# Kernel optimization log

Hardware: AMD Instinct MI355X
Metric: run time of the kernel (lower is better)

## Reference

```python
import jax, jax.numpy as jnp
import numpy as np

B, C_IN, T = 4, 256, 8192
LAYERS, STACKS = 24, 4
RES, GATE, SKIP, K = 128, 256, 128, 3
LPS = LAYERS // STACKS  # layers per stack -> dilation = 2**(i % LPS)
SQRT_HALF = 0.7071067811865476


def setup_inputs() -> dict:
    key = jax.random.key(0)
    ks = jax.random.split(key, 14)
    s = 0.08  # small init so the 24-layer stack stays well-scaled
    inp = {
        "x": jax.random.normal(ks[0], (B, C_IN, T), jnp.float32),
        "first_w": jax.random.normal(ks[1], (RES, C_IN), jnp.float32) * s,
        "first_b": jnp.zeros((RES,), jnp.float32),
        "conv_w": jax.random.normal(ks[2], (LAYERS, GATE, RES, K), jnp.float32) * s,
        "conv_b": jnp.zeros((LAYERS, GATE), jnp.float32),
        "out_w": jax.random.normal(ks[3], (LAYERS, RES, GATE // 2), jnp.float32) * s,
        "out_b": jnp.zeros((LAYERS, RES), jnp.float32),
        "skip_w": jax.random.normal(ks[4], (LAYERS, SKIP, GATE // 2), jnp.float32) * s,
        "skip_b": jnp.zeros((LAYERS, SKIP), jnp.float32),
        "last1_w": jax.random.normal(ks[5], (SKIP, SKIP), jnp.float32) * s,
        "last1_b": jnp.zeros((SKIP,), jnp.float32),
        "last2_w": jax.random.normal(ks[6], (C_IN, SKIP), jnp.float32) * s,
        "last2_b": jnp.zeros((C_IN,), jnp.float32),
    }
    return inp


def _conv1x1(w, b, h):
    # h: [B, C, T], w: [O, C]
    return jnp.einsum('oc,bct->bot', w, h) + b[None, :, None]


def _causal_dilated_conv(h, w, b, dilation):
    # left pad == torch symmetric pad (k-1)*d followed by crop to first T (causal)
    pad = (K - 1) * dilation
    hp = jnp.pad(h, ((0, 0), (0, 0), (pad, 0)))
    y = jax.lax.conv_general_dilated(
        hp, w, window_strides=(1,), padding='VALID',
        rhs_dilation=(dilation,), dimension_numbers=('NCH', 'OIH', 'NCH'))
    return y + b[None, :, None]


def reference(x, first_w, first_b, conv_w, conv_b, out_w, out_b,
              skip_w, skip_b, last1_w, last1_b, last2_w, last2_b):
    h = _conv1x1(first_w, first_b, x)  # [B, RES, T]
    skips = jnp.zeros((x.shape[0], SKIP, x.shape[-1]), h.dtype)
    for i in range(LAYERS):
        d = 2 ** (i % LPS)
        y = _causal_dilated_conv(h, conv_w[i], conv_b[i], d)  # [B, GATE, T]
        a, g = jnp.split(y, 2, axis=1)
        z = jnp.tanh(a) * jax.nn.sigmoid(g)  # gated tanh*sigmoid
        skips = skips + _conv1x1(skip_w[i], skip_b[i], z)
        h = (_conv1x1(out_w[i], out_b[i], z) + h) * SQRT_HALF  # residual
    skips = skips * (1.0 / LAYERS) ** 0.5
    out = jax.nn.relu(skips)
    out = jax.nn.relu(_conv1x1(last1_w, last1_b, out))
    out = _conv1x1(last2_w, last2_b, out)  # logits [B, 256, T]
    return out
```

## Files before the change

### kernel.cpp

```cpp
#include <hip/hip_runtime.h>

#define B 4
#define CIN 256
#define T 8192
#define NL 24
#define SH 0.70710678118654752f
#define SKIP_SCALE 0.20412414523193150f

typedef unsigned short u16;
typedef __attribute__((ext_vector_type(4))) float f32x4;
typedef __attribute__((ext_vector_type(8))) short s16x8;
typedef __attribute__((ext_vector_type(4))) short s16x4;

__device__ inline u16 f2bf(float f) {
  unsigned u = __float_as_uint(f);
  return (u16)((u + 0x7fffu + ((u >> 16) & 1u)) >> 16);
}
__device__ inline float gate_fn(float a, float g) {
  float e2 = __expf(-2.f * fabsf(a));
  float th = (1.f - e2) * __builtin_amdgcn_rcpf(1.f + e2);
  float sg = __builtin_amdgcn_rcpf(1.f + __expf(-g));
  return copysignf(th, a) * sg;
}

__global__ void cvt_all(const float* __restrict__ conv_w, const float* __restrict__ skip_w,
                        const float* __restrict__ out_w, const float* __restrict__ first_w,
                        const float* __restrict__ last1_w, const float* __restrict__ last2_w,
                        u16* __restrict__ wcv, u16* __restrict__ wso, u16* __restrict__ wf,
                        u16* __restrict__ w1, u16* __restrict__ w2) {
  int i = blockIdx.x * 256 + threadIdx.x;
  if (i < 2359296) {
    int c = i & 127, o = (i >> 7) & 255, kk = (i >> 15) % 3, l = (i >> 15) / 3;
    wcv[i] = f2bf(conv_w[(((size_t)l * 256 + o) * 128 + c) * 3 + kk]);
    return;
  }
  i -= 2359296;
  if (i < 786432) {
    int c = i & 127, r = (i >> 7) & 255, l = i >> 15;
    float v = (r < 128) ? skip_w[((size_t)l * 128 + r) * 128 + c]
                        : out_w[((size_t)l * 128 + (r - 128)) * 128 + c];
    wso[i] = f2bf(v);
    return;
  }
  i -= 786432;
  if (i < 32768) { wf[i] = f2bf(first_w[i]); return; }
  i -= 32768;
  if (i < 16384) { w1[i] = f2bf(last1_w[i]); return; }
  i -= 16384;
  if (i < 32768) { w2[i] = f2bf(last2_w[i]); return; }
}
__global__ void sumsb_kernel(const float* __restrict__ sb, float* __restrict__ dst) {
  int c = threadIdx.x;
  float s = 0.f;
  for (int l = 0; l < NL; l++) s += sb[l * 128 + c];
  dst[c] = s;
}

__global__ __launch_bounds__(256, 2)
void first_kernel(const float* __restrict__ x, const u16* __restrict__ wf,
                  const float* __restrict__ fb, float* __restrict__ hf) {
  __shared__ u16 xT[64 * 256];
  const int tid = threadIdx.x, wv = tid >> 6, lane = tid & 63, lo = lane & 15, hi = lane >> 4;
  const int t0 = blockIdx.x * 64, b = blockIdx.y;

  #pragma unroll
  for (int it = 0; it < 16; it++) {
    int idx = tid + it * 256;
    int c = idx >> 4, t4 = (idx & 15) << 2;
    f32x4 v = *(const f32x4*)(x + ((size_t)b * CIN + c) * T + t0 + t4);
    #pragma unroll
    for (int i = 0; i < 4; i++) {
      int t = t4 + i;
      *(u16*)((char*)xT + t * 512 + ((c * 2) ^ ((t & 7) << 4))) = f2bf(v[i]);
    }
  }
  __syncthreads();

  f32x4 acc[2][4];
  #pragma unroll
  for (int m = 0; m < 2; m++)
    #pragma unroll
    for (int n = 0; n < 4; n++) acc[m][n] = (f32x4){0.f, 0.f, 0.f, 0.f};
  #pragma unroll
  for (int s = 0; s < 8; s++) {
    s16x8 af[2], bf[4];
    #pragma unroll
    for (int m = 0; m < 2; m++)
      af[m] = *(const s16x8*)(wf + (size_t)(wv * 32 + m * 16 + lo) * CIN + s * 32 + hi * 8);
    #pragma unroll
    for (int n = 0; n < 4; n++) {
      int t = n * 16 + lo;
      bf[n] = *(const s16x8*)((const char*)xT + t * 512 + ((s * 64 + hi * 16) ^ ((t & 7) << 4)));
    }
    #pragma unroll
    for (int m = 0; m < 2; m++)
      #pragma unroll
      for (int n = 0; n < 4; n++)
        acc[m][n] = __builtin_amdgcn_mfma_f32_16x16x32_bf16(af[m], bf[n], acc[m][n], 0, 0, 0);
  }
  #pragma unroll
  for (int m = 0; m < 2; m++) {
    int c0 = wv * 32 + m * 16 + hi * 4;
    f32x4 bv = *(const f32x4*)(fb + c0);
    #pragma unroll
    for (int n = 0; n < 4; n++) {
      int t = n * 16 + lo;
      *(f32x4*)(hf + ((size_t)b * T + t0 + t) * 128 + c0) = acc[m][n] + bv;
    }
  }
}

__global__ __launch_bounds__(512, 4)
void pair_kernel(const float* __restrict__ hf_in, float* __restrict__ hf_out,
                 float* __restrict__ skip,
                 const u16* __restrict__ wc1, const float* __restrict__ cb1,
                 const u16* __restrict__ ws1, const float* __restrict__ ob1,
                 const u16* __restrict__ wc2, const float* __restrict__ cb2,
                 const u16* __restrict__ ws2, const float* __restrict__ ob2,
                 int d1, int d2, int first) {
  extern __shared__ u16 lds[];
  u16* h_s = lds;
  u16* zh  = lds + 160 * 128;
  const int tid = threadIdx.x, wv = tid >> 6, lane = tid & 63, lo = lane & 15, hi = lane >> 4;
  const int tj = blockIdx.x, b = blockIdx.y, t0 = tj * 64;
  const int R0 = 128 + 2 * d1;

  for (int p = tid; p < R0 * 32; p += 512) {
    int j0 = p >> 5, cq = p & 31;
    int t = t0 - 64 - 2 * d1 + j0;
    f32x4 v = (f32x4){0.f, 0.f, 0.f, 0.f};
    if (t >= 0) v = *(const f32x4*)(hf_in + ((size_t)b * T + t) * 128 + cq * 4);
    s16x4 pk;
    #pragma unroll
    for (int j = 0; j < 4; j++) pk[j] = (short)f2bf(v[j]);
    *(s16x4*)((char*)h_s + j0 * 256 + ((cq * 8) ^ (((j0 + 64 - 2 * d1) & 7) << 4))) = pk;
  }
  __syncthreads();

  f32x4 A[2][8];
  const int oa = wv * 16, og = 128 + wv * 16;

  #pragma unroll
  for (int m = 0; m < 2; m++)
    #pragma unroll
    for (int n = 0; n < 8; n++) A[m][n] = (f32x4){0.f, 0.f, 0.f, 0.f};
  #pragma unroll
  for (int k = 0; k < 3; k++) {
    const int st = ((lo + (k + 6) * d1) & 7) << 4;
    const int jb = k * d1;
    #pragma unroll
    for (int s = 0; s < 4; s++) {
      s16x8 af0 = *(const s16x8*)(wc1 + ((size_t)(k * 256 + oa + lo)) * 128 + s * 32 + hi * 8);
      s16x8 af1 = *(const s16x8*)(wc1 + ((size_t)(k * 256 + og + lo)) * 128 + s * 32 + hi * 8);
      const int cb_ = s * 64 + hi * 16;
      #pragma unroll
      for (int h2 = 0; h2 < 2; h2++) {
        s16x8 bf[4];
        #pragma unroll
        for (int nn = 0; nn < 4; nn++) {
          int j0 = (h2 * 4 + nn) * 16 + lo + jb;
          bf[nn] = *(const s16x8*)((const char*)h_s + j0 * 256 + (cb_ ^ st));
        }
        #pragma unroll
        for (int nn = 0; nn < 4; nn++) {
          A[0][h2 * 4 + nn] = __builtin_amdgcn_mfma_f32_16x16x32_bf16(af0, bf[nn], A[0][h2 * 4 + nn], 0, 0, 0);
          A[1][h2 * 4 + nn] = __builtin_amdgcn_mfma_f32_16x16x32_bf16(af1, bf[nn], A[1][h2 * 4 + nn], 0, 0, 0);
        }
      }
    }
  }
  {
    f32x4 ba = *(const f32x4*)(cb1 + oa + hi * 4);
    f32x4 bg = *(const f32x4*)(cb1 + og + hi * 4);
    #pragma unroll
    for (int n = 0; n < 8; n++) {
      int u = n * 16 + lo;
      s16x4 pk;
      #pragma unroll
      for (int j = 0; j < 4; j++)
        pk[j] = (short)f2bf(gate_fn(A[0][n][j] + ba[j], A[1][n][j] + bg[j]));
      *(s16x4*)((char*)zh + u * 256 + (((oa + hi * 4) * 2) ^ ((lo & 7) << 4))) = pk;
    }
  }
  __syncthreads();

  const int ro = wv * 32;
  if (wv < 4) {
    #pragma unroll
    for (int m = 0; m < 2; m++)
      #pragma unroll
      for (int nn = 0; nn < 4; nn++) A[m][nn + 4] = (f32x4){0.f, 0.f, 0.f, 0.f};
    #pragma unroll
    for (int s = 0; s < 4; s++) {
      s16x8 af0 = *(const s16x8*)(ws1 + (size_t)(ro + lo) * 128 + s * 32 + hi * 8);
      s16x8 af1 = *(const s16x8*)(ws1 + (size_t)(ro + 16 + lo) * 128 + s * 32 + hi * 8);
      const int cb_ = s * 64 + hi * 16;
      s16x8 bf[4];
      #pragma unroll
      for (int nn = 0; nn < 4; nn++) {
        int u = (nn + 4) * 16 + lo;
        bf[nn] = *(const s16x8*)((const char*)zh + u * 256 + (cb_ ^ ((lo & 7) << 4)));
      }
      #pragma unroll
      for (int nn = 0; nn < 4; nn++) {
        A[0][nn + 4] = __builtin_amdgcn_mfma_f32_16x16x32_bf16(af0, bf[nn], A[0][nn + 4], 0, 0, 0);
        A[1][nn + 4] = __builtin_amdgcn_mfma_f32_16x16x32_bf16(af1, bf[nn], A[1][nn + 4], 0, 0, 0);
      }
    }
  } else {
    #pragma unroll
    for (int m = 0; m < 2; m++)
      #pragma unroll
      for (int n = 0; n < 8; n++) A[m][n] = (f32x4){0.f, 0.f, 0.f, 0.f};
    #pragma unroll
    for (int s = 0; s < 4; s++) {
      s16x8 af0 = *(const s16x8*)(ws1 + (size_t)(ro + lo) * 128 + s * 32 + hi * 8);
      s16x8 af1 = *(const s16x8*)(ws1 + (size_t)(ro + 16 + lo) * 128 + s * 32 + hi * 8);
      const int cb_ = s * 64 + hi * 16;
      #pragma unroll
      for (int h2 = 0; h2 < 2; h2++) {
        s16x8 bf[4];
        #pragma unroll
        for (int nn = 0; nn < 4; nn++) {
          int u = (h2 * 4 + nn) * 16 + lo;
          bf[nn] = *(const s16x8*)((const char*)zh + u * 256 + (cb_ ^ ((lo & 7) << 4)));
        }
        #pragma unroll
        for (int nn = 0; nn < 4; nn++) {
          A[0][h2 * 4 + nn] = __builtin_amdgcn_mfma_f32_16x16x32_bf16(af0, bf[nn], A[0][h2 * 4 + nn], 0, 0, 0);
          A[1][h2 * 4 + nn] = __builtin_amdgcn_mfma_f32_16x16x32_bf16(af1, bf[nn], A[1][h2 * 4 + nn], 0, 0, 0);
        }
      }
    }
    #pragma unroll
    for (int m = 0; m < 2; m++) {
      int c0 = (wv - 4) * 32 + m * 16 + hi * 4;
      f32x4 ob4 = *(const f32x4*)(ob1 + c0);
      #pragma unroll
      for (int n = 0; n < 8; n++) {
        int u = n * 16 + lo;
        int t_out = t0 - 64 + u;
        f32x4 h0 = (f32x4){0.f, 0.f, 0.f, 0.f};
        if (t_out >= 0) h0 = *(const f32x4*)(hf_in + ((size_t)b * T + t_out) * 128 + c0);
        f32x4 h1 = (A[m][n] + ob4 + h0) * SH;
        if (t_out < 0) h1 = (f32x4){0.f, 0.f, 0.f, 0.f};
        A[m][n] = h1;
        s16x4 pk;
        #pragma unroll
        for (int j = 0; j < 4; j++) pk[j] = (short)f2bf(h1[j]);
        *(s16x4*)((char*)h_s + u * 256 + ((c0 * 2) ^ ((lo & 7) << 4))) = pk;
      }
    }
  }
  __syncthreads();

  #pragma unroll
  for (int m = 0; m < 2; m++)
    #pragma unroll
    for (int n = 0; n < 4; n++) A[m][n] = (f32x4){0.f, 0.f, 0.f, 0.f};
  #pragma unroll
  for (int k = 0; k < 3; k++) {
    const int st = ((lo + (k + 6) * d2) & 7) << 4;
    const int jb2 = 64 - 2 * d2 + k * d2;
    #pragma unroll
    for (int s = 0; s < 4; s++) {
      s16x8 af0 = *(const s16x8*)(wc2 + ((size_t)(k * 256 + oa + lo)) * 128 + s * 32 + hi * 8);
      s16x8 af1 = *(const s16x8*)(wc2 + ((size_t)(k * 256 + og + lo)) * 128 + s * 32 + hi * 8);
      const int cb_ = s * 64 + hi * 16;
      s16x8 bf[4];
      #pragma unroll
      for (int nn = 0; nn < 4; nn++) {
        int j1 = nn * 16 + lo + jb2;
        bf[nn] = *(const s16x8*)((const char*)h_s + j1 * 256 + (cb_ ^ st));
      }
      #pragma unroll
      for (int nn = 0; nn < 4; nn++) {
        A[0][nn] = __builtin_amdgcn_mfma_f32_16x16x32_bf16(af0, bf[nn], A[0][nn], 0, 0, 0);
        A[1][nn] = __builtin_amdgcn_mfma_f32_16x16x32_bf16(af1, bf[nn], A[1][nn], 0, 0, 0);
      }
    }
  }
  {
    f32x4 ba = *(const f32x4*)(cb2 + oa + hi * 4);
    f32x4 bg = *(const f32x4*)(cb2 + og + hi * 4);
    #pragma unroll
    for (int n = 0; n < 4; n++) {
      int u = n * 16 + lo;
      s16x4 pk;
      #pragma unroll
      for (int j = 0; j < 4; j++)
        pk[j] = (short)f2bf(gate_fn(A[0][n][j] + ba[j], A[1][n][j] + bg[j]));
      *(s16x4*)((char*)zh + u * 256 + (((oa + hi * 4) * 2) ^ ((lo & 7) << 4))) = pk;
    }
  }
  __syncthreads();

  if (wv < 4) {
    #pragma unroll
    for (int s = 0; s < 4; s++) {
      s16x8 af0 = *(const s16x8*)(ws2 + (size_t)(ro + lo) * 128 + s * 32 + hi * 8);
      s16x8 af1 = *(const s16x8*)(ws2 + (size_t)(ro + 16 + lo) * 128 + s * 32 + hi * 8);
      const int cb_ = s * 64 + hi * 16;
      s16x8 bf[4];
      #pragma unroll
      for (int nn = 0; nn < 4; nn++) {
        int u = nn * 16 + lo;
        bf[nn] = *(const s16x8*)((const char*)zh + u * 256 + (cb_ ^ ((lo & 7) << 4)));
      }
      #pragma unroll
      for (int nn = 0; nn < 4; nn++) {
        A[0][nn + 4] = __builtin_amdgcn_mfma_f32_16x16x32_bf16(af0, bf[nn], A[0][nn + 4], 0, 0, 0);
        A[1][nn + 4] = __builtin_amdgcn_mfma_f32_16x16x32_bf16(af1, bf[nn], A[1][nn + 4], 0, 0, 0);
      }
    }
    #pragma unroll
    for (int m = 0; m < 2; m++) {
      int c0 = ro + m * 16 + hi * 4;
      #pragma unroll
      for (int n = 0; n < 4; n++) {
        int t = t0 + n * 16 + lo;
        size_t off = ((size_t)b * T + t) * 128 + c0;
        f32x4 r = A[m][n + 4];
        if (!first) r += *(const f32x4*)(skip + off);
        *(f32x4*)(skip + off) = r;
      }
    }
  } else {
    #pragma unroll
    for (int m = 0; m < 2; m++)
      #pragma unroll
      for (int n = 0; n < 4; n++) A[m][n] = (f32x4){0.f, 0.f, 0.f, 0.f};
    #pragma unroll
    for (int s = 0; s < 4; s++) {
      s16x8 af0 = *(const s16x8*)(ws2 + (size_t)(ro + lo) * 128 + s * 32 + hi * 8);
      s16x8 af1 = *(const s16x8*)(ws2 + (size_t)(ro + 16 + lo) * 128 + s * 32 + hi * 8);
      const int cb_ = s * 64 + hi * 16;
      s16x8 bf[4];
      #pragma unroll
      for (int nn = 0; nn < 4; nn++) {
        int u = nn * 16 + lo;
        bf[nn] = *(const s16x8*)((const char*)zh + u * 256 + (cb_ ^ ((lo & 7) << 4)));
      }
      #pragma unroll
      for (int nn = 0; nn < 4; nn++) {
        A[0][nn] = __builtin_amdgcn_mfma_f32_16x16x32_bf16(af0, bf[nn], A[0][nn], 0, 0, 0);
        A[1][nn] = __builtin_amdgcn_mfma_f32_16x16x32_bf16(af1, bf[nn], A[1][nn], 0, 0, 0);
      }
    }
    #pragma unroll
    for (int m = 0; m < 2; m++) {
      int c0 = (wv - 4) * 32 + m * 16 + hi * 4;
      f32x4 ob4 = *(const f32x4*)(ob2 + c0);
      #pragma unroll
      for (int n = 0; n < 4; n++) {
        int t = t0 + n * 16 + lo;
        f32x4 h2v = (A[m][n] + ob4 + A[m][n + 4]) * SH;
        *(f32x4*)(hf_out + ((size_t)b * T + t) * 128 + c0) = h2v;
      }
    }
  }
}

__global__ __launch_bounds__(256, 2)
void head_kernel(const float* __restrict__ skip, const float* __restrict__ sumsb,
                 const u16* __restrict__ w1, const float* __restrict__ b1v,
                 const u16* __restrict__ w2, const float* __restrict__ b2v,
                 float* __restrict__ out) {
  __shared__ u16 sT[64 * 128];
  __shared__ u16 s1T[64 * 128];
  const int tid = threadIdx.x, wv = tid >> 6, lane = tid & 63, lo = lane & 15, hi = lane >> 4;
  const int t0 = blockIdx.x * 64, b = blockIdx.y;

  #pragma unroll
  for (int it = 0; it < 8; it++) {
    int p = tid + it * 256;
    int t = p >> 5, cq = p & 31;
    f32x4 v = *(const f32x4*)(skip + ((size_t)b * T + t0 + t) * 128 + cq * 4);
    f32x4 sb4 = *(const f32x4*)(sumsb + cq * 4);
    s16x4 pk;
    #pragma unroll
    for (int j = 0; j < 4; j++) pk[j] = (short)f2bf(fmaxf((v[j] + sb4[j]) * SKIP_SCALE, 0.f));
    *(s16x4*)((char*)sT + t * 256 + ((cq * 8) ^ ((t & 7) << 4))) = pk;
  }
  __syncthreads();
  {
    f32x4 acc[2][4];
    #pragma unroll
    for (int m = 0; m < 2; m++)
      #pragma unroll
      for (int n = 0; n < 4; n++) acc[m][n] = (f32x4){0.f, 0.f, 0.f, 0.f};
    #pragma unroll
    for (int s = 0; s < 4; s++) {
      s16x8 af0 = *(const s16x8*)(w1 + (size_t)(wv * 32 + lo) * 128 + s * 32 + hi * 8);
      s16x8 af1 = *(const s16x8*)(w1 + (size_t)(wv * 32 + 16 + lo) * 128 + s * 32 + hi * 8);
      #pragma unroll
      for (int n = 0; n < 4; n++) {
        int t = n * 16 + lo;
        s16x8 bf = *(const s16x8*)((const char*)sT + t * 256 + ((s * 64 + hi * 16) ^ ((t & 7) << 4)));
        acc[0][n] = __builtin_amdgcn_mfma_f32_16x16x32_bf16(af0, bf, acc[0][n], 0, 0, 0);
        acc[1][n] = __builtin_amdgcn_mfma_f32_16x16x32_bf16(af1, bf, acc[1][n], 0, 0, 0);
      }
    }
    #pragma unroll
    for (int m = 0; m < 2; m++) {
      int c0 = wv * 32 + m * 16 + hi * 4;
      f32x4 bv = *(const f32x4*)(b1v + c0);
      #pragma unroll
      for (int n = 0; n < 4; n++) {
        int t = n * 16 + lo;
        s16x4 pk;
        #pragma unroll
        for (int j = 0; j < 4; j++) pk[j] = (short)f2bf(fmaxf(acc[m][n][j] + bv[j], 0.f));
        *(s16x4*)((char*)s1T + t * 256 + ((c0 * 2) ^ ((t & 7) << 4))) = pk;
      }
    }
  }
  __syncthreads();
  {
    f32x4 acc[4][4];
    #pragma unroll
    for (int m = 0; m < 4; m++)
      #pragma unroll
      for (int n = 0; n < 4; n++) acc[m][n] = (f32x4){0.f, 0.f, 0.f, 0.f};
    #pragma unroll
    for (int s = 0; s < 4; s++) {
      s16x8 af[4];
      #pragma unroll
      for (int m = 0; m < 4; m++)
        af[m] = *(const s16x8*)(w2 + (size_t)(wv * 64 + m * 16 + lo) * 128 + s * 32 + hi * 8);
      #pragma unroll
      for (int n = 0; n < 4; n++) {
        int t = n * 16 + lo;
        s16x8 bf = *(const s16x8*)((const char*)s1T + t * 256 + ((s * 64 + hi * 16) ^ ((t & 7) << 4)));
        #pragma unroll
        for (int m = 0; m < 4; m++)
          acc[m][n] = __builtin_amdgcn_mfma_f32_16x16x32_bf16(af[m], bf, acc[m][n], 0, 0, 0);
      }
    }
    #pragma unroll
    for (int m = 0; m < 4; m++) {
      int c0 = wv * 64 + m * 16 + hi * 4;
      f32x4 bv = *(const f32x4*)(b2v + c0);
      #pragma unroll
      for (int n = 0; n < 4; n++) {
        int t = t0 + n * 16 + lo;
        f32x4 r = acc[m][n] + bv;
        #pragma unroll
        for (int j = 0; j < 4; j++) out[((size_t)b * CIN + c0 + j) * T + t] = r[j];
      }
    }
  }
}

extern "C" void kernel_launch(void* const* d_in, const int* in_sizes, int n_in,
                              void* d_out, int out_size, void* d_ws, size_t ws_size,
                              hipStream_t stream) {
  const float* x       = (const float*)d_in[0];
  const float* first_w = (const float*)d_in[1];
  const float* first_b = (const float*)d_in[2];
  const float* conv_w  = (const float*)d_in[3];
  const float* conv_b  = (const float*)d_in[4];
  const float* out_w   = (const float*)d_in[5];
  const float* out_b   = (const float*)d_in[6];
  const float* skip_w  = (const float*)d_in[7];
  const float* skip_b  = (const float*)d_in[8];
  const float* last1_w = (const float*)d_in[9];
  const float* last1_b = (const float*)d_in[10];
  const float* last2_w = (const float*)d_in[11];
  const float* last2_b = (const float*)d_in[12];
  float* out = (float*)d_out;

  u16* wcv = (u16*)d_ws;
  u16* wso = wcv + (size_t)NL * 3 * 256 * 128;
  u16* wf  = wso + (size_t)NL * 256 * 128;
  u16* w1  = wf + 128 * 256;
  u16* w2  = w1 + 128 * 128;
  float* sumsb = (float*)(w2 + 256 * 128);
  float* skipF = sumsb + 128;
  float* hfA = (float*)d_out;
  float* hfB = hfA + (size_t)B * T * 128;

  cvt_all<<<12608, 256, 0, stream>>>(conv_w, skip_w, out_w, first_w, last1_w, last2_w,
                                     wcv, wso, wf, w1, w2);
  sumsb_kernel<<<1, 128, 0, stream>>>(skip_b, sumsb);

  dim3 grid(T / 64, B);
  first_kernel<<<grid, 256, 0, stream>>>(x, wf, first_b, hfA);

  for (int p = 0; p < NL / 2; p++) {
    int l1 = 2 * p, l2 = 2 * p + 1;
    int d1 = 1 << (l1 % 6), d2 = 1 << (l2 % 6);
    const float* hin = (p & 1) ? hfB : hfA;
    float* hout = (p & 1) ? hfA : hfB;
    pair_kernel<<<grid, 512, 73728, stream>>>(
        hin, hout, skipF,
        wcv + (size_t)l1 * 3 * 256 * 128, conv_b + (size_t)l1 * 256,
        wso + (size_t)l1 * 256 * 128, out_b + (size_t)l1 * 128,
        wcv + (size_t)l2 * 3 * 256 * 128, conv_b + (size_t)l2 * 256,
        wso + (size_t)l2 * 256 * 128, out_b + (size_t)l2 * 128,
        d1, d2, p == 0 ? 1 : 0);
  }
  head_kernel<<<grid, 256, 0, stream>>>(skipF, sumsb, w1, last1_b, w2, last2_b, out);
}
```

Before: 696.8 us.

## Fuse whole WaveNet into one persistent cooperative kernel with grid syncs

Replaces the per-pair kernel launches, first and head kernels with a single cooperative kernel of 256 blocks. Each block keeps its 128-timestep tile of the residual and skip state in registers across all 24 layers and exchanges only the causal halo rows through a small bf16 global buffer, separated by grid-wide syncs. This is meant to remove launch overhead and the full-tensor float round trips of the hidden state between layers. It adds 24 grid barriers, runs only one block per CU on 256 CUs, and falls back to the old multi-kernel path if the cooperative launch fails.

```diff
diff --git a/kernel.cpp b/kernel.cpp
--- a/kernel.cpp
+++ b/kernel.cpp
@@ -1,4 +1,7 @@
 #include <hip/hip_runtime.h>
+#include <hip/hip_cooperative_groups.h>
+
+namespace cg = cooperative_groups;
 
 #define B 4
 #define CIN 256
@@ -8,6 +11,7 @@
 #define SKIP_SCALE 0.20412414523193150f
 
 typedef unsigned short u16;
+typedef unsigned long long u64;
 typedef __attribute__((ext_vector_type(4))) float f32x4;
 typedef __attribute__((ext_vector_type(8))) short s16x8;
 typedef __attribute__((ext_vector_type(4))) short s16x4;
@@ -56,13 +60,270 @@
   dst[c] = s;
 }
 
+__global__ __launch_bounds__(512, 2)
+void wavenet_kernel(const float* __restrict__ x,
+                    const u16* __restrict__ wf, const float* __restrict__ fb,
+                    const u16* __restrict__ wcv, const float* __restrict__ cbv,
+                    const u16* __restrict__ wso, const float* __restrict__ obv,
+                    const u16* __restrict__ w1, const float* __restrict__ b1,
+                    const u16* __restrict__ w2, const float* __restrict__ b2,
+                    const float* __restrict__ sumsb,
+                    u16* __restrict__ hG0, u16* __restrict__ hG1,
+                    float* __restrict__ out)
+{
+  cg::grid_group gg = cg::this_grid();
+  extern __shared__ char smem[];
+  u16* h_s = (u16*)smem;
+  u16* zh  = (u16*)(smem + 49152);
+  u16* xT  = (u16*)smem;
+  const int tid = threadIdx.x, wv = tid >> 6, lane = tid & 63, lo = lane & 15, hi = lane >> 4;
+  const int bid = blockIdx.x, tj = bid & 63, b = bid >> 6, t0 = tj * 128;
+
+  f32x4 res[2][8];
+  f32x4 acc[2][8];
+  #pragma unroll
+  for (int m = 0; m < 2; m++)
+    #pragma unroll
+    for (int n = 0; n < 8; n++) res[m][n] = (f32x4){0.f, 0.f, 0.f, 0.f};
+
+  #pragma unroll
+  for (int it = 0; it < 16; it++) {
+    int idx = tid + it * 512;
+    int c = idx >> 5, t4 = (idx & 31) << 2;
+    f32x4 v = *(const f32x4*)(x + ((size_t)b * CIN + c) * T + t0 + t4);
+    #pragma unroll
+    for (int j = 0; j < 4; j++) {
+      int t = t4 + j;
+      *(u16*)((char*)xT + t * 512 + ((c * 2) ^ ((t & 7) << 4))) = f2bf(v[j]);
+    }
+  }
+  __syncthreads();
+  if (wv >= 4) {
+    #pragma unroll
+    for (int m = 0; m < 2; m++)
+      #pragma unroll
+      for (int n = 0; n < 8; n++) acc[m][n] = (f32x4){0.f, 0.f, 0.f, 0.f};
+    #pragma unroll
+    for (int s = 0; s < 8; s++) {
+      s16x8 af0 = *(const s16x8*)(wf + (size_t)((wv - 4) * 32 + lo) * CIN + s * 32 + hi * 8);
+      s16x8 af1 = *(const s16x8*)(wf + (size_t)((wv - 4) * 32 + 16 + lo) * CIN + s * 32 + hi * 8);
+      #pragma unroll
+      for (int n = 0; n < 8; n++) {
+        int t = n * 16 + lo;
+        s16x8 bf = *(const s16x8*)((const char*)xT + t * 512 + ((s * 64 + hi * 16) ^ ((t & 7) << 4)));
+        acc[0][n] = __builtin_amdgcn_mfma_f32_16x16x32_bf16(af0, bf, acc[0][n], 0, 0, 0);
+        acc[1][n] = __builtin_amdgcn_mfma_f32_16x16x32_bf16(af1, bf, acc[1][n], 0, 0, 0);
+      }
+    }
+    #pragma unroll
+    for (int m = 0; m < 2; m++) {
+      f32x4 fb4 = *(const f32x4*)(fb + (wv - 4) * 32 + m * 16 + hi * 4);
+      #pragma unroll
+      for (int n = 0; n < 8; n++) res[m][n] = acc[m][n] + fb4;
+    }
+  }
+  __syncthreads();
+
+  #pragma unroll 1
+  for (int i = 0; i < NL; i++) {
+    const int d = 1 << (i % 6);
+    const u16* wc = wcv + (size_t)i * 3 * 256 * 128;
+    const float* cb = cbv + i * 256;
+    const u16* wsl = wso + (size_t)i * 256 * 128;
+    const float* ob = obv + i * 128;
+    u16* hG = (i & 1) ? hG1 : hG0;
+
+    if (wv >= 4) {
+      #pragma unroll
+      for (int m = 0; m < 2; m++) {
+        int c0 = (wv - 4) * 32 + m * 16 + hi * 4;
+        #pragma unroll
+        for (int n = 0; n < 8; n++) {
+          int tl = n * 16 + lo;
+          s16x4 pk;
+          #pragma unroll
+          for (int j = 0; j < 4; j++) pk[j] = (short)f2bf(res[m][n][j]);
+          *(s16x4*)((char*)h_s + (2 * d + tl) * 256 + ((c0 * 2) ^ ((tl & 7) << 4))) = pk;
+          if (tl >= 128 - 2 * d && tj < 63)
+            *(u64*)(hG + ((size_t)(b * 64 + tj) * 64 + (tl - 64)) * 128 + c0) = *(const u64*)&pk;
+        }
+      }
+    }
+    gg.sync();
+    for (int p = tid; p < 64 * d; p += 512) {
+      int r = p >> 5, cq = p & 31;
+      u64 v = 0;
+      if (tj > 0)
+        v = *(const u64*)(hG + ((size_t)(b * 64 + tj - 1) * 64 + (64 - 2 * d + r)) * 128 + cq * 4);
+      *(u64*)((char*)h_s + r * 256 + ((cq * 8) ^ (((r + 6 * d) & 7) << 4))) = v;
+    }
+    __syncthreads();
+
+    #pragma unroll
+    for (int m = 0; m < 2; m++)
+      #pragma unroll
+      for (int n = 0; n < 8; n++) acc[m][n] = (f32x4){0.f, 0.f, 0.f, 0.f};
+    const int oa = wv * 16, og = 128 + wv * 16;
+    #pragma unroll
+    for (int k = 0; k < 3; k++) {
+      const int jb = k * d;
+      const int st = ((lo + (k + 6) * d) & 7) << 4;
+      #pragma unroll
+      for (int s = 0; s < 4; s++) {
+        s16x8 af0 = *(const s16x8*)(wc + ((size_t)(k * 256 + oa + lo)) * 128 + s * 32 + hi * 8);
+        s16x8 af1 = *(const s16x8*)(wc + ((size_t)(k * 256 + og + lo)) * 128 + s * 32 + hi * 8);
+        const int cbyte = s * 64 + hi * 16;
+        #pragma unroll
+        for (int n = 0; n < 8; n++) {
+          int j = n * 16 + lo + jb;
+          s16x8 bf = *(const s16x8*)((const char*)h_s + j * 256 + (cbyte ^ st));
+          acc[0][n] = __builtin_amdgcn_mfma_f32_16x16x32_bf16(af0, bf, acc[0][n], 0, 0, 0);
+          acc[1][n] = __builtin_amdgcn_mfma_f32_16x16x32_bf16(af1, bf, acc[1][n], 0, 0, 0);
+        }
+      }
+    }
+    {
+      f32x4 ba = *(const f32x4*)(cb + oa + hi * 4);
+      f32x4 bg = *(const f32x4*)(cb + og + hi * 4);
+      #pragma unroll
+      for (int n = 0; n < 8; n++) {
+        int tl = n * 16 + lo;
+        s16x4 pk;
+        #pragma unroll
+        for (int j = 0; j < 4; j++)
+          pk[j] = (short)f2bf(gate_fn(acc[0][n][j] + ba[j], acc[1][n][j] + bg[j]));
+        *(s16x4*)((char*)zh + tl * 256 + (((oa + hi * 4) * 2) ^ ((tl & 7) << 4))) = pk;
+      }
+    }
+    __syncthreads();
+
+    const int ro = wv * 32;
+    if (wv < 4) {
+      #pragma unroll
+      for (int s = 0; s < 4; s++) {
+        s16x8 af0 = *(const s16x8*)(wsl + (size_t)(ro + lo) * 128 + s * 32 + hi * 8);
+        s16x8 af1 = *(const s16x8*)(wsl + (size_t)(ro + 16 + lo) * 128 + s * 32 + hi * 8);
+        const int cbyte = s * 64 + hi * 16;
+        #pragma unroll
+        for (int n = 0; n < 8; n++) {
+          int tl = n * 16 + lo;
+          s16x8 bf = *(const s16x8*)((const char*)zh + tl * 256 + (cbyte ^ ((tl & 7) << 4)));
+          res[0][n] = __builtin_amdgcn_mfma_f32_16x16x32_bf16(af0, bf, res[0][n], 0, 0, 0);
+          res[1][n] = __builtin_amdgcn_mfma_f32_16x16x32_bf16(af1, bf, res[1][n], 0, 0, 0);
+        }
+      }
+    } else {
+      #pragma unroll
+      for (int m = 0; m < 2; m++)
+        #pragma unroll
+        for (int n = 0; n < 8; n++) acc[m][n] = (f32x4){0.f, 0.f, 0.f, 0.f};
+      #pragma unroll
+      for (int s = 0; s < 4; s++) {
+        s16x8 af0 = *(const s16x8*)(wsl + (size_t)(ro + lo) * 128 + s * 32 + hi * 8);
+        s16x8 af1 = *(const s16x8*)(wsl + (size_t)(ro + 16 + lo) * 128 + s * 32 + hi * 8);
+        const int cbyte = s * 64 + hi * 16;
+        #pragma unroll
+        for (int n = 0; n < 8; n++) {
+          int tl = n * 16 + lo;
+          s16x8 bf = *(const s16x8*)((const char*)zh + tl * 256 + (cbyte ^ ((tl & 7) << 4)));
+          acc[0][n] = __builtin_amdgcn_mfma_f32_16x16x32_bf16(af0, bf, acc[0][n], 0, 0, 0);
+          acc[1][n] = __builtin_amdgcn_mfma_f32_16x16x32_bf16(af1, bf, acc[1][n], 0, 0, 0);
+        }
+      }
+      #pragma unroll
+      for (int m = 0; m < 2; m++) {
+        f32x4 ob4 = *(const f32x4*)(ob + (ro - 128) + m * 16 + hi * 4);
+        #pragma unroll
+        for (int n = 0; n < 8; n++)
+          res[m][n] = (acc[m][n] + ob4 + res[m][n]) * SH;
+      }
+    }
+    __syncthreads();
+  }
+  gg.sync();
+
+  if (wv < 4) {
+    #pragma unroll
+    for (int m = 0; m < 2; m++) {
+      int c0 = wv * 32 + m * 16 + hi * 4;
+      f32x4 sv = *(const f32x4*)(sumsb + c0);
+      #pragma unroll
+      for (int n = 0; n < 8; n++) {
+        int tl = n * 16 + lo;
+        s16x4 pk;
+        #pragma unroll
+        for (int j = 0; j < 4; j++)
+          pk[j] = (short)f2bf(fmaxf((res[m][n][j] + sv[j]) * SKIP_SCALE, 0.f));
+        *(s16x4*)((char*)h_s + tl * 256 + ((c0 * 2) ^ ((tl & 7) << 4))) = pk;
+      }
+    }
+  }
+  __syncthreads();
+  {
+    f32x4 a1[8];
+    #pragma unroll
+    for (int n = 0; n < 8; n++) a1[n] = (f32x4){0.f, 0.f, 0.f, 0.f};
+    #pragma unroll
+    for (int s = 0; s < 4; s++) {
+      s16x8 af = *(const s16x8*)(w1 + (size_t)(wv * 16 + lo) * 128 + s * 32 + hi * 8);
+      #pragma unroll
+      for (int n = 0; n < 8; n++) {
+        int tl = n * 16 + lo;
+        s16x8 bf = *(const s16x8*)((const char*)h_s + tl * 256 + ((s * 64 + hi * 16) ^ ((tl & 7) << 4)));
+        a1[n] = __builtin_amdgcn_mfma_f32_16x16x32_bf16(af, bf, a1[n], 0, 0, 0);
+      }
+    }
+    int c0 = wv * 16 + hi * 4;
+    f32x4 b14 = *(const f32x4*)(b1 + c0);
+    #pragma unroll
+    for (int n = 0; n < 8; n++) {
+      int tl = n * 16 + lo;
+      s16x4 pk;
+      #pragma unroll
+      for (int j = 0; j < 4; j++) pk[j] = (short)f2bf(fmaxf(a1[n][j] + b14[j], 0.f));
+      *(s16x4*)((char*)zh + tl * 256 + ((c0 * 2) ^ ((tl & 7) << 4))) = pk;
+    }
+  }
+  __syncthreads();
+  {
+    const int ro = wv * 32;
+    #pragma unroll
+    for (int m = 0; m < 2; m++)
+      #pragma unroll
+      for (int n = 0; n < 8; n++) acc[m][n] = (f32x4){0.f, 0.f, 0.f, 0.f};
+    #pragma unroll
+    for (int s = 0; s < 4; s++) {
+      s16x8 af0 = *(const s16x8*)(w2 + (size_t)(ro + lo) * 128 + s * 32 + hi * 8);
+      s16x8 af1 = *(const s16x8*)(w2 + (size_t)(ro + 16 + lo) * 128 + s * 32 + hi * 8);
+      #pragma unroll
+      for (int n = 0; n < 8; n++) {
+        int tl = n * 16 + lo;
+        s16x8 bf = *(const s16x8*)((const char*)zh + tl * 256 + ((s * 64 + hi * 16) ^ ((tl & 7) << 4)));
+        acc[0][n] = __builtin_amdgcn_mfma_f32_16x16x32_bf16(af0, bf, acc[0][n], 0, 0, 0);
+        acc[1][n] = __builtin_amdgcn_mfma_f32_16x16x32_bf16(af1, bf, acc[1][n], 0, 0, 0);
+      }
+    }
+    #pragma unroll
+    for (int m = 0; m < 2; m++) {
+      int c0 = ro + m * 16 + hi * 4;
+      f32x4 b24 = *(const f32x4*)(b2 + c0);
+      #pragma unroll
+      for (int n = 0; n < 8; n++) {
+        int t = t0 + n * 16 + lo;
+        #pragma unroll
+        for (int j = 0; j < 4; j++)
+          out[((size_t)b * CIN + c0 + j) * T + t] = acc[m][n][j] + b24[j];
+      }
+    }
+  }
+}
+
 __global__ __launch_bounds__(256, 2)
 void first_kernel(const float* __restrict__ x, const u16* __restrict__ wf,
                   const float* __restrict__ fb, float* __restrict__ hf) {
   __shared__ u16 xT[64 * 256];
   const int tid = threadIdx.x, wv = tid >> 6, lane = tid & 63, lo = lane & 15, hi = lane >> 4;
   const int t0 = blockIdx.x * 64, b = blockIdx.y;
-
   #pragma unroll
   for (int it = 0; it < 16; it++) {
     int idx = tid + it * 256;
@@ -75,7 +336,6 @@
     }
   }
   __syncthreads();
-
   f32x4 acc[2][4];
   #pragma unroll
   for (int m = 0; m < 2; m++)
@@ -468,37 +728,48 @@
   const float* last1_b = (const float*)d_in[10];
   const float* last2_w = (const float*)d_in[11];
   const float* last2_b = (const float*)d_in[12];
-  float* out = (float*)d_out;
+  float* outp = (float*)d_out;
 
   u16* wcv = (u16*)d_ws;
   u16* wso = wcv + (size_t)NL * 3 * 256 * 128;
-  u16* wf  = wso + (size_t)NL * 256 * 128;
-  u16* w1  = wf + 128 * 256;
-  u16* w2  = w1 + 128 * 128;
-  float* sumsb = (float*)(w2 + 256 * 128);
+  u16* wfB = wso + (size_t)NL * 256 * 128;
+  u16* w1B = wfB + 128 * 256;
+  u16* w2B = w1B + 128 * 128;
+  float* sumsb = (float*)(w2B + 256 * 128);
   float* skipF = sumsb + 128;
-  float* hfA = (float*)d_out;
-  float* hfB = hfA + (size_t)B * T * 128;
+  u16* hG0 = (u16*)((char*)d_out + (size_t)24 * 1024 * 1024);
+  u16* hG1 = hG0 + (size_t)B * 64 * 64 * 128;
 
   cvt_all<<<12608, 256, 0, stream>>>(conv_w, skip_w, out_w, first_w, last1_w, last2_w,
-                                     wcv, wso, wf, w1, w2);
+                                     wcv, wso, wfB, w1B, w2B);
   sumsb_kernel<<<1, 128, 0, stream>>>(skip_b, sumsb);
 
-  dim3 grid(T / 64, B);
-  first_kernel<<<grid, 256, 0, stream>>>(x, wf, first_b, hfA);
-
-  for (int p = 0; p < NL / 2; p++) {
-    int l1 = 2 * p, l2 = 2 * p + 1;
-    int d1 = 1 << (l1 % 6), d2 = 1 << (l2 % 6);
-    const float* hin = (p & 1) ? hfB : hfA;
-    float* hout = (p & 1) ? hfA : hfB;
-    pair_kernel<<<grid, 512, 73728, stream>>>(
-        hin, hout, skipF,
-        wcv + (size_t)l1 * 3 * 256 * 128, conv_b + (size_t)l1 * 256,
-        wso + (size_t)l1 * 256 * 128, out_b + (size_t)l1 * 128,
-        wcv + (size_t)l2 * 3 * 256 * 128, conv_b + (size_t)l2 * 256,
-        wso + (size_t)l2 * 256 * 128, out_b + (size_t)l2 * 128,
-        d1, d2, p == 0 ? 1 : 0);
-  }
-  head_kernel<<<grid, 256, 0, stream>>>(skipF, sumsb, w1, last1_b, w2, last2_b, out);
-}
+  void* kargs[] = {(void*)&x, (void*)&wfB, (void*)&first_b,
+                   (void*)&wcv, (void*)&conv_b, (void*)&wso, (void*)&out_b,
+                   (void*)&w1B, (void*)&last1_b, (void*)&w2B, (void*)&last2_b,
+                   (void*)&sumsb, (void*)&hG0, (void*)&hG1, (void*)&outp};
+  hipError_t ce = hipLaunchCooperativeKernel((const void*)wavenet_kernel,
+                                             dim3(256), dim3(512), kargs,
+                                             81920, stream);
+  if (ce != hipSuccess) {
+    (void)hipGetLastError();
+    float* hfA = (float*)d_out;
+    float* hfB = hfA + (size_t)B * T * 128;
+    dim3 grid(T / 64, B);
+    first_kernel<<<grid, 256, 0, stream>>>(x, wfB, first_b, hfA);
+    for (int p = 0; p < NL / 2; p++) {
+      int l1 = 2 * p, l2 = 2 * p + 1;
+      int d1 = 1 << (l1 % 6), d2 = 1 << (l2 % 6);
+      const float* hin = (p & 1) ? hfB : hfA;
+      float* hout = (p & 1) ? hfA : hfB;
+      pair_kernel<<<grid, 512, 73728, stream>>>(
+          hin, hout, skipF,
+          wcv + (size_t)l1 * 3 * 256 * 128, conv_b + (size_t)l1 * 256,
+          wso + (size_t)l1 * 256 * 128, out_b + (size_t)l1 * 128,
+          wcv + (size_t)l2 * 3 * 256 * 128, conv_b + (size_t)l2 * 256,
+          wso + (size_t)l2 * 256 * 128, out_b + (size_t)l2 * 128,
+          d1, d2, p == 0 ? 1 : 0);
+    }
+    head_kernel<<<grid, 256, 0, stream>>>(skipF, sumsb, w1B, last1_b, w2B, last2_b, outp);
+  }
+}
```

Measured after the change: 1.083 ms. 55.5% more time.

## Fuse each six-layer dilation stack into one kernel with LDS halo

Applied to the files above, without the earlier changes.

Adds a group_kernel that runs a whole stack of six dilated layers per block over a 128-step tile, with a 128-step left halo held in LDS. The residual is kept as a hi/lo bf16 pair so it stays close to fp32 precision, and halo regions are skipped where the receptive field no longer needs them. This replaces twelve pair launches with four launches and removes most global round-trips of the residual stream. In exchange it recomputes the halo, uses 144KB of LDS with only 256 blocks, and falls back to pair_kernel if the launch fails.

```diff
diff --git a/kernel.cpp b/kernel.cpp
--- a/kernel.cpp
+++ b/kernel.cpp
@@ -16,6 +16,7 @@
   unsigned u = __float_as_uint(f);
   return (u16)((u + 0x7fffu + ((u >> 16) & 1u)) >> 16);
 }
+__device__ inline float bf2f(u16 h) { return __uint_as_float((unsigned)h << 16); }
 __device__ inline float gate_fn(float a, float g) {
   float e2 = __expf(-2.f * fabsf(a));
   float th = (1.f - e2) * __builtin_amdgcn_rcpf(1.f + e2);
@@ -62,7 +63,6 @@
   __shared__ u16 xT[64 * 256];
   const int tid = threadIdx.x, wv = tid >> 6, lane = tid & 63, lo = lane & 15, hi = lane >> 4;
   const int t0 = blockIdx.x * 64, b = blockIdx.y;
-
   #pragma unroll
   for (int it = 0; it < 16; it++) {
     int idx = tid + it * 256;
@@ -75,7 +75,6 @@
     }
   }
   __syncthreads();
-
   f32x4 acc[2][4];
   #pragma unroll
   for (int m = 0; m < 2; m++)
@@ -106,6 +105,199 @@
     for (int n = 0; n < 4; n++) {
       int t = n * 16 + lo;
       *(f32x4*)(hf + ((size_t)b * T + t0 + t) * 128 + c0) = acc[m][n] + bv;
+    }
+  }
+}
+
+__global__ __launch_bounds__(512, 2)
+void group_kernel(const float* __restrict__ hf_in, float* __restrict__ hf_out,
+                  float* __restrict__ skip,
+                  const u16* __restrict__ wcv_g, const float* __restrict__ cb_g,
+                  const u16* __restrict__ wso_g, const float* __restrict__ ob_g,
+                  int first) {
+  extern __shared__ char smem[];
+  u16* hHI = (u16*)smem;
+  u16* hLO = (u16*)(smem + 65536);
+  u16* zh  = (u16*)(smem + 131072);
+  const int tid = threadIdx.x, wv = tid >> 6, lane = tid & 63, lo = lane & 15, hi = lane >> 4;
+  const int tj = blockIdx.x & 63, b = blockIdx.x >> 6, t0 = tj * 128;
+
+  #pragma unroll
+  for (int it = 0; it < 16; it++) {
+    int p = tid + it * 512;
+    int r = p >> 5, cq = p & 31;
+    int t = t0 - 128 + r;
+    f32x4 v = (f32x4){0.f, 0.f, 0.f, 0.f};
+    if (t >= 0) v = *(const f32x4*)(hf_in + ((size_t)b * T + t) * 128 + cq * 4);
+    s16x4 phi, plo;
+    #pragma unroll
+    for (int q = 0; q < 4; q++) {
+      u16 hb = f2bf(v[q]);
+      phi[q] = (short)hb;
+      plo[q] = (short)f2bf(v[q] - bf2f(hb));
+    }
+    int off = r * 256 + ((cq * 8) ^ ((r & 7) << 4));
+    *(s16x4*)((char*)hHI + off) = phi;
+    *(s16x4*)((char*)hLO + off) = plo;
+  }
+  __syncthreads();
+
+  f32x4 sk[2][8];
+  #pragma unroll
+  for (int m = 0; m < 2; m++)
+    #pragma unroll
+    for (int n = 0; n < 8; n++) sk[m][n] = (f32x4){0.f, 0.f, 0.f, 0.f};
+
+  #pragma unroll 1
+  for (int j = 0; j < 6; j++) {
+    const int d = 1 << j;
+    const u16* wc = wcv_g + (size_t)j * 3 * 256 * 128;
+    const float* cb = cb_g + j * 256;
+    const u16* wsl = wso_g + (size_t)j * 256 * 128;
+    const float* ob = ob_g + j * 128;
+    const int cmin = (j == 5) ? 2 : (j == 4) ? 1 : 0;
+
+    #pragma unroll
+    for (int ci = 0; ci < 4; ci++) {
+      const int c = 3 - ci;
+      if (c < cmin) continue;
+
+      f32x4 acc[2][4];
+      #pragma unroll
+      for (int m = 0; m < 2; m++)
+        #pragma unroll
+        for (int n = 0; n < 4; n++) acc[m][n] = (f32x4){0.f, 0.f, 0.f, 0.f};
+      const int oa = wv * 16, og = 128 + wv * 16;
+      #pragma unroll
+      for (int k = 0; k < 3; k++) {
+        const int rb = 64 * c - (2 - k) * d + lo;
+        #pragma unroll
+        for (int s = 0; s < 4; s++) {
+          s16x8 af0 = *(const s16x8*)(wc + (size_t)(k * 256 + oa + lo) * 128 + s * 32 + hi * 8);
+          s16x8 af1 = *(const s16x8*)(wc + (size_t)(k * 256 + og + lo) * 128 + s * 32 + hi * 8);
+          const int cbyte = s * 64 + hi * 16;
+          s16x8 bfr[4];
+          #pragma unroll
+          for (int n = 0; n < 4; n++) {
+            int rr = rb + n * 16;
+            if (rr < 0) rr = 0;
+            bfr[n] = *(const s16x8*)((const char*)hHI + rr * 256 + (cbyte ^ ((rr & 7) << 4)));
+          }
+          #pragma unroll
+          for (int n = 0; n < 4; n++) {
+            acc[0][n] = __builtin_amdgcn_mfma_f32_16x16x32_bf16(af0, bfr[n], acc[0][n], 0, 0, 0);
+            acc[1][n] = __builtin_amdgcn_mfma_f32_16x16x32_bf16(af1, bfr[n], acc[1][n], 0, 0, 0);
+          }
+        }
+      }
+      {
+        f32x4 ba = *(const f32x4*)(cb + oa + hi * 4);
+        f32x4 bg = *(const f32x4*)(cb + og + hi * 4);
+        #pragma unroll
+        for (int n = 0; n < 4; n++) {
+          int u = n * 16 + lo;
+          s16x4 pk;
+          #pragma unroll
+          for (int q = 0; q < 4; q++)
+            pk[q] = (short)f2bf(gate_fn(acc[0][n][q] + ba[q], acc[1][n][q] + bg[q]));
+          *(s16x4*)((char*)zh + u * 256 + (((oa + hi * 4) * 2) ^ ((u & 7) << 4))) = pk;
+        }
+      }
+      __syncthreads();
+
+      if (wv < 4) {
+        if (c >= 2) {
+          const int ro = wv * 32;
+          #pragma unroll
+          for (int s = 0; s < 4; s++) {
+            s16x8 af0 = *(const s16x8*)(wsl + (size_t)(ro + lo) * 128 + s * 32 + hi * 8);
+            s16x8 af1 = *(const s16x8*)(wsl + (size_t)(ro + 16 + lo) * 128 + s * 32 + hi * 8);
+            const int cbyte = s * 64 + hi * 16;
+            s16x8 bfr[4];
+            #pragma unroll
+            for (int n = 0; n < 4; n++) {
+              int u = n * 16 + lo;
+              bfr[n] = *(const s16x8*)((const char*)zh + u * 256 + (cbyte ^ ((u & 7) << 4)));
+            }
+            #pragma unroll
+            for (int n = 0; n < 4; n++) {
+              sk[0][(c - 2) * 4 + n] = __builtin_amdgcn_mfma_f32_16x16x32_bf16(af0, bfr[n], sk[0][(c - 2) * 4 + n], 0, 0, 0);
+              sk[1][(c - 2) * 4 + n] = __builtin_amdgcn_mfma_f32_16x16x32_bf16(af1, bfr[n], sk[1][(c - 2) * 4 + n], 0, 0, 0);
+            }
+          }
+        }
+      } else {
+        const int ro = (wv - 4) * 32;
+        f32x4 a2[2][4];
+        #pragma unroll
+        for (int m = 0; m < 2; m++)
+          #pragma unroll
+          for (int n = 0; n < 4; n++) a2[m][n] = (f32x4){0.f, 0.f, 0.f, 0.f};
+        #pragma unroll
+        for (int s = 0; s < 4; s++) {
+          s16x8 af0 = *(const s16x8*)(wsl + (size_t)(128 + ro + lo) * 128 + s * 32 + hi * 8);
+          s16x8 af1 = *(const s16x8*)(wsl + (size_t)(128 + ro + 16 + lo) * 128 + s * 32 + hi * 8);
+          const int cbyte = s * 64 + hi * 16;
+          s16x8 bfr[4];
+          #pragma unroll
+          for (int n = 0; n < 4; n++) {
+            int u = n * 16 + lo;
+            bfr[n] = *(const s16x8*)((const char*)zh + u * 256 + (cbyte ^ ((u & 7) << 4)));
+          }
+          #pragma unroll
+          for (int n = 0; n < 4; n++) {
+            a2[0][n] = __builtin_amdgcn_mfma_f32_16x16x32_bf16(af0, bfr[n], a2[0][n], 0, 0, 0);
+            a2[1][n] = __builtin_amdgcn_mfma_f32_16x16x32_bf16(af1, bfr[n], a2[1][n], 0, 0, 0);
+          }
+        }
+        #pragma unroll
+        for (int m = 0; m < 2; m++) {
+          int c0 = ro + m * 16 + hi * 4;
+          f32x4 ob4 = *(const f32x4*)(ob + c0);
+          #pragma unroll
+          for (int n = 0; n < 4; n++) {
+            int u = n * 16 + lo;
+            int r = 64 * c + u;
+            int off = r * 256 + ((c0 * 2) ^ ((r & 7) << 4));
+            s16x4 vhi = *(const s16x4*)((const char*)hHI + off);
+            s16x4 vlo = *(const s16x4*)((const char*)hLO + off);
+            f32x4 hold;
+            #pragma unroll
+            for (int q = 0; q < 4; q++)
+              hold[q] = bf2f((u16)vhi[q]) + bf2f((u16)vlo[q]);
+            f32x4 hnew = (a2[m][n] + ob4 + hold) * SH;
+            if (j == 5) {
+              *(f32x4*)(hf_out + ((size_t)b * T + t0 + (r - 128)) * 128 + c0) = hnew;
+            } else {
+              s16x4 nhi, nlo;
+              #pragma unroll
+              for (int q = 0; q < 4; q++) {
+                u16 hb = f2bf(hnew[q]);
+                nhi[q] = (short)hb;
+                nlo[q] = (short)f2bf(hnew[q] - bf2f(hb));
+              }
+              *(s16x4*)((char*)hHI + off) = nhi;
+              *(s16x4*)((char*)hLO + off) = nlo;
+            }
+          }
+        }
+      }
+      __syncthreads();
+    }
+  }
+
+  if (wv < 4) {
+    #pragma unroll
+    for (int m = 0; m < 2; m++) {
+      int c0 = wv * 32 + m * 16 + hi * 4;
+      #pragma unroll
+      for (int nn = 0; nn < 8; nn++) {
+        int t = t0 + nn * 16 + lo;
+        size_t off = ((size_t)b * T + t) * 128 + c0;
+        f32x4 r = sk[m][nn];
+        if (!first) r += *(const f32x4*)(skip + off);
+        *(f32x4*)(skip + off) = r;
+      }
     }
   }
 }
@@ -468,37 +660,56 @@
   const float* last1_b = (const float*)d_in[10];
   const float* last2_w = (const float*)d_in[11];
   const float* last2_b = (const float*)d_in[12];
-  float* out = (float*)d_out;
+  float* outp = (float*)d_out;
 
   u16* wcv = (u16*)d_ws;
   u16* wso = wcv + (size_t)NL * 3 * 256 * 128;
-  u16* wf  = wso + (size_t)NL * 256 * 128;
-  u16* w1  = wf + 128 * 256;
-  u16* w2  = w1 + 128 * 128;
-  float* sumsb = (float*)(w2 + 256 * 128);
+  u16* wfB = wso + (size_t)NL * 256 * 128;
+  u16* w1B = wfB + 128 * 256;
+  u16* w2B = w1B + 128 * 128;
+  float* sumsb = (float*)(w2B + 256 * 128);
   float* skipF = sumsb + 128;
   float* hfA = (float*)d_out;
   float* hfB = hfA + (size_t)B * T * 128;
 
   cvt_all<<<12608, 256, 0, stream>>>(conv_w, skip_w, out_w, first_w, last1_w, last2_w,
-                                     wcv, wso, wf, w1, w2);
+                                     wcv, wso, wfB, w1B, w2B);
   sumsb_kernel<<<1, 128, 0, stream>>>(skip_b, sumsb);
 
-  dim3 grid(T / 64, B);
-  first_kernel<<<grid, 256, 0, stream>>>(x, wf, first_b, hfA);
-
-  for (int p = 0; p < NL / 2; p++) {
-    int l1 = 2 * p, l2 = 2 * p + 1;
-    int d1 = 1 << (l1 % 6), d2 = 1 << (l2 % 6);
-    const float* hin = (p & 1) ? hfB : hfA;
-    float* hout = (p & 1) ? hfA : hfB;
-    pair_kernel<<<grid, 512, 73728, stream>>>(
-        hin, hout, skipF,
-        wcv + (size_t)l1 * 3 * 256 * 128, conv_b + (size_t)l1 * 256,
-        wso + (size_t)l1 * 256 * 128, out_b + (size_t)l1 * 128,
-        wcv + (size_t)l2 * 3 * 256 * 128, conv_b + (size_t)l2 * 256,
-        wso + (size_t)l2 * 256 * 128, out_b + (size_t)l2 * 128,
-        d1, d2, p == 0 ? 1 : 0);
-  }
-  head_kernel<<<grid, 256, 0, stream>>>(skipF, sumsb, w1, last1_b, w2, last2_b, out);
-}
+  dim3 g64(T / 64, B);
+  first_kernel<<<g64, 256, 0, stream>>>(x, wfB, first_b, hfA);
+
+  (void)hipFuncSetAttribute((const void*)group_kernel,
+                            hipFuncAttributeMaxDynamicSharedMemorySize, 147456);
+  (void)hipGetLastError();
+
+  group_kernel<<<dim3(256), dim3(512), 147456, stream>>>(
+      hfA, hfB, skipF, wcv, conv_b, wso, out_b, 1);
+  hipError_t ce = hipGetLastError();
+
+  if (ce == hipSuccess) {
+    for (int g = 1; g < 4; g++) {
+      const float* hin = (g & 1) ? hfB : hfA;
+      float* hout = (g & 1) ? hfA : hfB;
+      group_kernel<<<dim3(256), dim3(512), 147456, stream>>>(
+          hin, hout, skipF,
+          wcv + (size_t)g * 6 * 3 * 256 * 128, conv_b + (size_t)g * 6 * 256,
+          wso + (size_t)g * 6 * 256 * 128, out_b + (size_t)g * 6 * 128, 0);
+    }
+  } else {
+    for (int p = 0; p < NL / 2; p++) {
+      int l1 = 2 * p, l2 = 2 * p + 1;
+      int d1 = 1 << (l1 % 6), d2 = 1 << (l2 % 6);
+      const float* hin = (p & 1) ? hfB : hfA;
+      float* hout = (p & 1) ? hfA : hfB;
+      pair_kernel<<<g64, 512, 73728, stream>>>(
+          hin, hout, skipF,
+          wcv + (size_t)l1 * 3 * 256 * 128, conv_b + (size_t)l1 * 256,
+          wso + (size_t)l1 * 256 * 128, out_b + (size_t)l1 * 128,
+          wcv + (size_t)l2 * 3 * 256 * 128, conv_b + (size_t)l2 * 256,
+          wso + (size_t)l2 * 256 * 128, out_b + (size_t)l2 * 128,
+          d1, d2, p == 0 ? 1 : 0);
+    }
+  }
+  head_kernel<<<g64, 256, 0, stream>>>(skipF, sumsb, w1B, last1_b, w2B, last2_b, outp);
+}
```

After: 865.0 us. +24.1%, slower.

## Keep a pre-swizzled bf16 copy of h and DMA it straight into LDS

Applied to the files above, without the earlier changes.

The first and pair kernels now also write a bf16 copy of the residual stream h, stored in the XOR-swizzled row layout that the pair kernel's LDS tile expects. The pair kernel fills its halo tile from that copy with global_load_lds 16-byte transfers, replacing fp32 global loads plus per-element bf16 conversion and swizzled LDS stores. Tiles at the start of the sequence, which need zero padding, fall back to a plain vector load path. This halves the bytes read for the input tile and moves the copy off the VALU, at the cost of an extra bf16 store of h per pair and more workspace.

```diff
diff --git a/kernel.cpp b/kernel.cpp
--- a/kernel.cpp
+++ b/kernel.cpp
@@ -21,6 +21,11 @@
   float th = (1.f - e2) * __builtin_amdgcn_rcpf(1.f + e2);
   float sg = __builtin_amdgcn_rcpf(1.f + __expf(-g));
   return copysignf(th, a) * sg;
+}
+__device__ inline void gload_lds16(const void* g, void* l) {
+  __builtin_amdgcn_global_load_lds(
+      (const __attribute__((address_space(1))) unsigned*)g,
+      (__attribute__((address_space(3))) unsigned*)l, 16, 0, 0);
 }
 
 __global__ void cvt_all(const float* __restrict__ conv_w, const float* __restrict__ skip_w,
@@ -58,11 +63,11 @@
 
 __global__ __launch_bounds__(256, 2)
 void first_kernel(const float* __restrict__ x, const u16* __restrict__ wf,
-                  const float* __restrict__ fb, float* __restrict__ hf) {
+                  const float* __restrict__ fb, float* __restrict__ hf,
+                  u16* __restrict__ sh) {
   __shared__ u16 xT[64 * 256];
   const int tid = threadIdx.x, wv = tid >> 6, lane = tid & 63, lo = lane & 15, hi = lane >> 4;
   const int t0 = blockIdx.x * 64, b = blockIdx.y;
-
   #pragma unroll
   for (int it = 0; it < 16; it++) {
     int idx = tid + it * 256;
@@ -75,7 +80,6 @@
     }
   }
   __syncthreads();
-
   f32x4 acc[2][4];
   #pragma unroll
   for (int m = 0; m < 2; m++)
@@ -104,14 +108,20 @@
     f32x4 bv = *(const f32x4*)(fb + c0);
     #pragma unroll
     for (int n = 0; n < 4; n++) {
-      int t = n * 16 + lo;
-      *(f32x4*)(hf + ((size_t)b * T + t0 + t) * 128 + c0) = acc[m][n] + bv;
+      int t = t0 + n * 16 + lo;
+      f32x4 h = acc[m][n] + bv;
+      *(f32x4*)(hf + ((size_t)b * T + t) * 128 + c0) = h;
+      s16x4 pk;
+      #pragma unroll
+      for (int j = 0; j < 4; j++) pk[j] = (short)f2bf(h[j]);
+      *(s16x4*)(sh + ((size_t)b * T + t) * 128 + (c0 ^ ((lo & 7) << 3))) = pk;
     }
   }
 }
 
 __global__ __launch_bounds__(512, 4)
 void pair_kernel(const float* __restrict__ hf_in, float* __restrict__ hf_out,
+                 const u16* __restrict__ sh_in, u16* __restrict__ sh_out,
                  float* __restrict__ skip,
                  const u16* __restrict__ wc1, const float* __restrict__ cb1,
                  const u16* __restrict__ ws1, const float* __restrict__ ob1,
@@ -124,16 +134,20 @@
   const int tid = threadIdx.x, wv = tid >> 6, lane = tid & 63, lo = lane & 15, hi = lane >> 4;
   const int tj = blockIdx.x, b = blockIdx.y, t0 = tj * 64;
   const int R0 = 128 + 2 * d1;
-
-  for (int p = tid; p < R0 * 32; p += 512) {
-    int j0 = p >> 5, cq = p & 31;
-    int t = t0 - 64 - 2 * d1 + j0;
-    f32x4 v = (f32x4){0.f, 0.f, 0.f, 0.f};
-    if (t >= 0) v = *(const f32x4*)(hf_in + ((size_t)b * T + t) * 128 + cq * 4);
-    s16x4 pk;
-    #pragma unroll
-    for (int j = 0; j < 4; j++) pk[j] = (short)f2bf(v[j]);
-    *(s16x4*)((char*)h_s + j0 * 256 + ((cq * 8) ^ (((j0 + 64 - 2 * d1) & 7) << 4))) = pk;
+  const int base_t = t0 - 64 - 2 * d1;
+
+  if (base_t >= 0) {
+    const char* src = (const char*)(sh_in + ((size_t)b * T + base_t) * 128);
+    for (int rr = wv * 4; rr < R0; rr += 32)
+      gload_lds16(src + rr * 256 + lane * 16, (char*)h_s + rr * 256);
+  } else {
+    for (int p = tid; p < R0 * 16; p += 512) {
+      int r = p >> 4, q = p & 15;
+      int t = base_t + r;
+      s16x8 v = (s16x8){0, 0, 0, 0, 0, 0, 0, 0};
+      if (t >= 0) v = *(const s16x8*)(sh_in + ((size_t)b * T + t) * 128 + q * 8);
+      *(s16x8*)((char*)h_s + r * 256 + q * 16) = v;
+    }
   }
   __syncthreads();
 
@@ -356,6 +370,10 @@
         int t = t0 + n * 16 + lo;
         f32x4 h2v = (A[m][n] + ob4 + A[m][n + 4]) * SH;
         *(f32x4*)(hf_out + ((size_t)b * T + t) * 128 + c0) = h2v;
+        s16x4 pk;
+        #pragma unroll
+        for (int j = 0; j < 4; j++) pk[j] = (short)f2bf(h2v[j]);
+        *(s16x4*)(sh_out + ((size_t)b * T + t) * 128 + (c0 ^ ((lo & 7) << 3))) = pk;
       }
     }
   }
@@ -468,37 +486,42 @@
   const float* last1_b = (const float*)d_in[10];
   const float* last2_w = (const float*)d_in[11];
   const float* last2_b = (const float*)d_in[12];
-  float* out = (float*)d_out;
-
+  float* outp = (float*)d_out;
+
+  const size_t NBT = (size_t)B * T * 128;
   u16* wcv = (u16*)d_ws;
   u16* wso = wcv + (size_t)NL * 3 * 256 * 128;
-  u16* wf  = wso + (size_t)NL * 256 * 128;
-  u16* w1  = wf + 128 * 256;
-  u16* w2  = w1 + 128 * 128;
-  float* sumsb = (float*)(w2 + 256 * 128);
+  u16* wfB = wso + (size_t)NL * 256 * 128;
+  u16* w1B = wfB + 128 * 256;
+  u16* w2B = w1B + 128 * 128;
+  float* sumsb = (float*)(w2B + 256 * 128);
   float* skipF = sumsb + 128;
+  u16* shA = (u16*)(skipF + NBT);
+  u16* shB = shA + NBT + 1024;
   float* hfA = (float*)d_out;
-  float* hfB = hfA + (size_t)B * T * 128;
+  float* hfB = hfA + NBT;
 
   cvt_all<<<12608, 256, 0, stream>>>(conv_w, skip_w, out_w, first_w, last1_w, last2_w,
-                                     wcv, wso, wf, w1, w2);
+                                     wcv, wso, wfB, w1B, w2B);
   sumsb_kernel<<<1, 128, 0, stream>>>(skip_b, sumsb);
 
-  dim3 grid(T / 64, B);
-  first_kernel<<<grid, 256, 0, stream>>>(x, wf, first_b, hfA);
+  dim3 g64(T / 64, B);
+  first_kernel<<<g64, 256, 0, stream>>>(x, wfB, first_b, hfA, shA);
 
   for (int p = 0; p < NL / 2; p++) {
     int l1 = 2 * p, l2 = 2 * p + 1;
     int d1 = 1 << (l1 % 6), d2 = 1 << (l2 % 6);
     const float* hin = (p & 1) ? hfB : hfA;
     float* hout = (p & 1) ? hfA : hfB;
-    pair_kernel<<<grid, 512, 73728, stream>>>(
-        hin, hout, skipF,
+    const u16* shin = (p & 1) ? shB : shA;
+    u16* shout = (p & 1) ? shA : shB;
+    pair_kernel<<<g64, 512, 73728, stream>>>(
+        hin, hout, shin, shout, skipF,
         wcv + (size_t)l1 * 3 * 256 * 128, conv_b + (size_t)l1 * 256,
         wso + (size_t)l1 * 256 * 128, out_b + (size_t)l1 * 128,
         wcv + (size_t)l2 * 3 * 256 * 128, conv_b + (size_t)l2 * 256,
         wso + (size_t)l2 * 256 * 128, out_b + (size_t)l2 * 128,
         d1, d2, p == 0 ? 1 : 0);
   }
-  head_kernel<<<grid, 256, 0, stream>>>(skipF, sumsb, w1, last1_b, w2, last2_b, out);
-}
+  head_kernel<<<g64, 256, 0, stream>>>(skipF, sumsb, w1B, last1_b, w2B, last2_b, outp);
+}
```

New measurement: 700.5 us. About the same (+0.5%).
